# Kernel optimization log

Hardware: AMD Instinct MI355X
Metric: run time of the kernel (lower is better)

## Reference

```python
import jax, jax.numpy as jnp
from jax import lax
import numpy as np

B, A, T = 128, 32, 32
HID = 64
DEG = 7
MODES = 25
OUT_FRAMES = 12
NHEAD, DHEAD = 16, 64


def legendre_tmat(out_frames, degree):
    # normalized Legendre basis evaluated at t_n, shape [degree+1, len(t_n)]
    t = np.arange(-6, out_frames + 1, dtype=np.float32)
    t = t / t[-1]
    P = [np.ones_like(t), t]
    for n in range(1, degree):
        P.append(((2 * n + 1) * t * P[n] - n * P[n - 1]) / (n + 1))
    P = np.stack(P[: degree + 1], 0)
    norm = np.sqrt((2 * np.arange(degree + 1) + 1) / 2.0).astype(np.float32)
    return (P * norm[:, None]).astype(np.float32)


def _conv(x, w, stride, pad):
    return lax.conv_general_dilated(x, w, (stride, stride), [(pad, pad), (pad, pad)],
                                    dimension_numbers=("NCHW", "OIHW", "NCHW"))


def _bn(x, g, b, eps=1e-5):
    m = jnp.mean(x, axis=(0, 2, 3), keepdims=True)
    v = jnp.var(x, axis=(0, 2, 3), keepdims=True)
    return (x - m) / jnp.sqrt(v + eps) * g[None, :, None, None] + b[None, :, None, None]


def setup_inputs() -> dict:
    key = jax.random.key(0)
    ks = jax.random.split(key, 32)

    def rn(i, shape, scale=0.05):
        return jax.random.normal(ks[i], shape, dtype=jnp.float32) * scale

    inp = {
        "cnn_feat": rn(0, (B, 1024, 14, 14), 1.0),
        "ego_state": rn(1, (B, T, 5), 1.0),
        "agents_state": rn(2, (B, A, T, 5), 1.0),
        "ego_state_len": jax.random.randint(ks[3], (B,), 0, T),
        "agents_state_len": jax.random.randint(ks[4], (B, A), 0, T),
        "agents_grid_pos": jax.random.randint(ks[5], (B, A, 2), 0, 14),
        "state_fc_W": rn(6, (HID, 5)), "state_fc_b": rn(7, (HID,)),
        "lstm_Wih": rn(8, (4 * HID, HID)), "lstm_Whh": rn(9, (4 * HID, HID)),
        "lstm_bih": rn(10, (4 * HID,)), "lstm_bhh": rn(11, (4 * HID,)),
        "enc_fc_W": rn(12, (HID, HID)), "enc_fc_b": rn(13, (HID,)),
        "conv1_W": rn(14, (512, 1024 + HID, 3, 3)),
        "bn1_g": jnp.ones((512,), jnp.float32), "bn1_b": jnp.zeros((512,), jnp.float32),
        "conv2_W": rn(15, (512, 512, 3, 3)),
        "bn2_g": jnp.ones((512,), jnp.float32), "bn2_b": jnp.zeros((512,), jnp.float32),
        "q_W": rn(16, (NHEAD * DHEAD, 512 + HID)),
        "k_W": rn(17, (NHEAD * DHEAD, 512, 1, 1)),
        "v_W": rn(18, (NHEAD * DHEAD, 512, 1, 1)),
        "attn_out_W": rn(19, (512, NHEAD * DHEAD)), "attn_out_b": rn(20, (512,)),
        "cls_W": rn(21, (MODES, 512 + HID + 512)), "cls_b": rn(22, (MODES,)),
        "dec1_W": rn(23, (256, 512 + HID + 512)), "dec1_b": rn(24, (256,)),
        "dec2_W": rn(25, ((DEG + 1) * 2 * MODES, 256)), "dec2_b": rn(26, ((DEG + 1) * 2 * MODES,)),
    }
    return inp


def reference(cnn_feat, ego_state, agents_state, ego_state_len, agents_state_len,
              agents_grid_pos, state_fc_W, state_fc_b, lstm_Wih, lstm_Whh, lstm_bih,
              lstm_bhh, enc_fc_W, enc_fc_b, conv1_W, bn1_g, bn1_b, conv2_W, bn2_g,
              bn2_b, q_W, k_W, v_W, attn_out_W, attn_out_b, cls_W, cls_b, dec1_W,
              dec1_b, dec2_W, dec2_b):
    Bn, _, Hs, Ws = cnn_feat.shape

    def lstm_encode(seq, lens):
        # seq [N,T,5]; packed-sequence semantics with zero init == take h at step len-1
        N, Tn, _ = seq.shape
        h = seq @ state_fc_W.T + state_fc_b  # [N,T,64]

        def step(carry, xt):
            hh, cc = carry
            g = xt @ lstm_Wih.T + hh @ lstm_Whh.T + lstm_bih + lstm_bhh
            i, f_, gg, o = jnp.split(g, 4, axis=-1)
            cc = jax.nn.sigmoid(f_) * cc + jax.nn.sigmoid(i) * jnp.tanh(gg)
            hh = jax.nn.sigmoid(o) * jnp.tanh(cc)
            return (hh, cc), hh

        z = jnp.zeros((N, HID), h.dtype)
        _, hs = lax.scan(step, (z, z), h.transpose(1, 0, 2))  # hs [T,N,64]
        idx = jnp.clip(lens, 1, Tn).astype(jnp.int32) - 1
        last = hs[idx, jnp.arange(N)]
        return last @ enc_fc_W.T + enc_fc_b

    ego = lstm_encode(ego_state, ego_state_len)  # [B,64]
    ag = lstm_encode(agents_state.reshape(Bn * A, T, 5),
                     agents_state_len.reshape(-1)).reshape(Bn, A, HID)

    # scatter-add agent encodings into the spatial grid (overlapping writes accumulate)
    grid = jnp.zeros((Bn, Hs, Ws, HID), cnn_feat.dtype)
    bidx = jnp.broadcast_to(jnp.arange(Bn)[:, None], (Bn, A))
    grid = grid.at[bidx, agents_grid_pos[..., 0], agents_grid_pos[..., 1]].add(ag)

    x = jnp.concatenate([cnn_feat, grid.transpose(0, 3, 1, 2)], axis=1)
    x = jax.nn.relu(_bn(_conv(x, conv1_W, 1, 1), bn1_g, bn1_b))
    x = jax.nn.relu(_bn(_conv(x, conv2_W, 2, 1), bn2_g, bn2_b))  # [B,512,7,7]

    ego_t = jnp.concatenate([x[:, :, 3, 3], ego], axis=1)  # [B,576]
    q = (ego_t @ q_W.T).reshape(Bn, NHEAD, DHEAD)
    k = _conv(x, k_W, 1, 1).reshape(Bn, NHEAD, DHEAD, -1)  # g = 9*9 = 81
    v = _conv(x, v_W, 1, 1).reshape(Bn, NHEAD, DHEAD, -1)
    energy = jnp.einsum("bhf,bhfg->bhg", q, k)
    attn = jax.nn.softmax(energy / (NHEAD * DHEAD) ** 0.5, axis=2)
    o = jnp.einsum("bhg,bhdg->bhd", attn, v).reshape(Bn, -1)
    o = o @ attn_out_W.T + attn_out_b

    feat = jnp.concatenate([o, ego_t], axis=1)  # [B,1088]
    conf = feat @ cls_W.T + cls_b
    d = jax.nn.relu(feat @ dec1_W.T + dec1_b)
    d = (d @ dec2_W.T + dec2_b).reshape(Bn, MODES, -1)

    tmat = jnp.asarray(legendre_tmat(OUT_FRAMES, DEG))  # [DEG+1, 19]
    out_x = d[:, :, : DEG + 1] @ tmat
    out_y = d[:, :, DEG + 1:] @ tmat
    traj = jnp.stack([out_x, out_y], axis=3)  # [B,MODES,19,2]
    return traj, conf
```

## Files before the change

### kernel.cpp

```cpp
#include <hip/hip_runtime.h>
#include <stdint.h>
#include <stddef.h>

#define DEVINL static __device__ __forceinline__

typedef __attribute__((ext_vector_type(8))) short  bfrag;
typedef __attribute__((ext_vector_type(4))) float  facc;

DEVINL uint16_t f2b(float f){
  uint32_t u = __float_as_uint(f);
  return (uint16_t)((u + 0x7fffu + ((u >> 16) & 1u)) >> 16);
}
DEVINL float b2f(uint16_t b){ return __uint_as_float(((uint32_t)b) << 16); }

DEVINL facc MFMA(bfrag a, bfrag b, facc c){
  return __builtin_amdgcn_mfma_f32_16x16x32_bf16(a, b, c, 0, 0, 0);
}

DEVINL void gload16(const void* g, void* l){
  __builtin_amdgcn_global_load_lds(
      (const __attribute__((address_space(1))) uint32_t*)g,
      (__attribute__((address_space(3))) uint32_t*)l, 16, 0, 0);
}

DEVINL float fast_tanh(float x){
  return 2.f/(1.f+__expf(-2.f*x)) - 1.f;
}

struct PrepArgs {
  const float* cnn;        uint16_t* Xp;
  uint16_t* Y1P;           float* gridb;   float* stats;
  const float *Wih, *Whh, *bih, *bhh, *sW, *sb, *encW;
  uint16_t* Wc;  float* be;  uint16_t* encWb;  float* tm;
  const float* conv1W;     uint16_t* WP1;
  const float* conv2W;     uint16_t* WP2;
  const float* kWf;        uint16_t* WKT;
  const float* fs[6];      uint16_t* fd[6];   int fn[6];  int fb0[6];
};

__global__ __launch_bounds__(256) void k_prep(PrepArgs a){
  int blk = blockIdx.x, t = threadIdx.x;
  if(blk < 4096){
    __shared__ float tile[32*200];
    int b = blk>>5, ch = blk&31;
    int c0 = ch*32;
    for(int i=t;i<32*196;i+=256){
      int ci = i/196, s = i%196;
      tile[ci*200+s] = a.cnn[((size_t)b*1024 + c0+ci)*196 + s];
    }
    __syncthreads();
    for(int i=t;i<16*196;i+=256){
      int s = i>>4, c2 = i&15;
      int y = s/14, x = s%14;
      uint32_t pu = (uint32_t)f2b(tile[(2*c2)*200+s]) |
                    ((uint32_t)f2b(tile[(2*c2+1)*200+s])<<16);
      *(uint32_t*)(a.Xp + (((size_t)b*16 + y+1)*16 + x+1)*1088 + c0 + 2*c2) = pu;
    }
  } else if(blk < 4352){
    int idx = blk - 4096;
    int b = idx & 127;
    uint16_t* base = (idx < 128) ? a.Xp : a.Y1P;
    int C = (idx < 128) ? 1088 : 512;
    for(int p=0;p<60;p++){
      int y, x;
      if(p<16){ y=0; x=p; }
      else if(p<32){ y=15; x=p-16; }
      else { int q=p-32; y=1+(q>>1); x=(q&1)?15:0; }
      uint32_t* dst = (uint32_t*)(base + ((size_t)(b*16+y)*16 + x)*C);
      for(int i=t;i<C/2;i+=256) dst[i] = 0;
    }
    float* g = a.gridb + (size_t)idx*6272;
    for(int i=t;i<6272;i+=256) g[i] = 0.f;
    if(idx == 0){
      for(int i=t;i<2048;i+=256) a.stats[i] = 0.f;
    }
  } else if(blk == 4352){
    int n = t;
    if(n < 19){
      float tv = (float)(n - 6) / 12.0f;
      float Pm = 1.0f, Pc = tv;
      a.tm[0*19+n] = Pm * sqrtf(0.5f);
      a.tm[1*19+n] = Pc * sqrtf(1.5f);
      for(int q=1; q<7; q++){
        float Pn = ((float)(2*q+1)*tv*Pc - (float)q*Pm) / (float)(q+1);
        Pm = Pc; Pc = Pn;
        a.tm[(q+1)*19+n] = Pc * sqrtf((float)(2*(q+1)+1) * 0.5f);
      }
    }
    for(int k=0;k<64;k++) a.Wc[n*96+k] = f2b(a.Whh[n*64+k]);
    for(int k5=0;k5<5;k5++){
      float s = 0.f;
      for(int j=0;j<64;j++) s += a.Wih[n*64+j]*a.sW[j*5+k5];
      a.Wc[n*96+64+k5] = f2b(s);
    }
    for(int k=69;k<96;k++) a.Wc[n*96+k] = 0;
    float s = 0.f;
    for(int j=0;j<64;j++) s += a.Wih[n*64+j]*a.sb[j];
    a.be[n] = s + a.bih[n] + a.bhh[n];
    if(n < 64){
      for(int k=0;k<64;k++) a.encWb[n*64+k] = f2b(a.encW[n*64+k]);
    }
  } else if(blk < 4865){
    int o = blk - 4353;
    for(int c=t; c<1088; c+=256){
      const float* src = a.conv1W + ((size_t)o*1088 + c)*9;
      float v[9];
      #pragma unroll
      for(int d=0;d<9;d++) v[d] = src[d];
      #pragma unroll
      for(int d=0;d<9;d++)
        a.WP1[((size_t)d*512 + o)*1088 + c] = f2b(v[d]);
    }
  } else if(blk < 5377){
    int o = blk - 4865;
    for(int c=t; c<512; c+=256){
      const float* src = a.conv2W + ((size_t)o*512 + c)*9;
      float v[9];
      #pragma unroll
      for(int d=0;d<9;d++) v[d] = src[d];
      #pragma unroll
      for(int dy=0;dy<3;dy++)
        #pragma unroll
        for(int dx=0;dx<3;dx++)
          a.WP2[((size_t)(dy*512 + o))*1536 + dx*512 + c] = f2b(v[dy*3+dx]);
    }
  } else if(blk < 5393){
    int h = blk - 5377;
    for(int i=t; i<32768; i+=256){
      int c = i>>6, d = i&63;
      a.WKT[((size_t)h*512 + c)*64 + d] = f2b(a.kWf[((size_t)(h*64+d))*512 + c]);
    }
  } else {
    int fblk = blk - 5393;
    int j = 0;
    while(j < 5 && fblk >= a.fb0[j+1]) j++;
    int base = (fblk - a.fb0[j])*8192;
    const float* s = a.fs[j];
    uint16_t* d = a.fd[j];
    int n = a.fn[j];
    int hi = base + 8192; if(hi > n) hi = n;
    for(int i=base+t; i<hi; i+=256) d[i] = f2b(s[i]);
  }
}

__global__ void k_packx_grid(const float* __restrict__ agrid, uint16_t* __restrict__ Xp)
{
  int b = blockIdx.x >> 1, half = blockIdx.x & 1;
  int j0 = half*32, t = threadIdx.x;
  for(int i=t;i<16*196;i+=256){
    int s = i>>4, j2 = i&15;
    int y = s/14, x = s%14;
    const float* gsrc = agrid + ((size_t)b*196 + s)*64 + j0 + 2*j2;
    uint32_t pu = (uint32_t)f2b(gsrc[0]) | ((uint32_t)f2b(gsrc[1])<<16);
    *(uint32_t*)(Xp + (((size_t)b*16 + y+1)*16 + x+1)*1088 + 1024 + j0 + 2*j2) = pu;
  }
}

__global__ __launch_bounds__(256) void k_lstm(
    const float* __restrict__ ego_seq, const float* __restrict__ ag_seq,
    const int* __restrict__ ego_len, const int* __restrict__ ag_len,
    const int* __restrict__ grid_pos,
    const uint16_t* __restrict__ Wc, const float* __restrict__ be,
    const uint16_t* __restrict__ encWb, const float* __restrict__ encB,
    float* __restrict__ agrid, uint16_t* __restrict__ egoT, uint16_t* __restrict__ feat)
{
  __shared__ __align__(16) uint16_t A[32*96];
  __shared__ float Xf[32*160];
  __shared__ int   idxs[32];

  int t = threadIdx.x, w = t>>6, l = t&63;
  int blk = blockIdx.x;
  bool isEgo = blk < 4;
  int seq0 = isEgo ? blk*32 : (blk-4)*32;
  const float* seqp = (isEgo ? ego_seq : ag_seq) + (size_t)seq0*160;

  for(int i=t;i<32*160;i+=256) Xf[i] = seqp[i];
  if(t < 32){
    int L = isEgo ? ego_len[seq0+t] : ag_len[seq0+t];
    if(L < 1) L = 1;
    idxs[t] = L-1;
  }
  for(int i=t;i<32*96;i+=256) A[i] = 0;

  bfrag bf[4][3];
  float be4[4];
  for(int ct=0;ct<4;ct++){
    int n = (ct*4+w)*16 + (l&15);
    for(int ks=0;ks<3;ks++)
      bf[ct][ks] = *(const bfrag*)(Wc + n*96 + ks*32 + (l>>4)*8);
    be4[ct] = be[n];
  }
  float cst[8], hl[8];
  for(int i=0;i<8;i++){ cst[i]=0.f; hl[i]=0.f; }
  __syncthreads();
  int myidx[8];
  for(int rt=0;rt<2;rt++) for(int r=0;r<4;r++){
    int s = rt*16 + (l>>4)*4 + r;
    myidx[rt*4+r] = idxs[s];
  }

  for(int st=0; st<32; st++){
    if(t < 160){ int s=t/5, kk=t%5; A[s*96+64+kk] = f2b(Xf[s*160 + st*5 + kk]); }
    __syncthreads();
    facc acc[2][4];
    for(int rt=0;rt<2;rt++) for(int ct=0;ct<4;ct++) acc[rt][ct] = facc{0.f,0.f,0.f,0.f};
    #pragma unroll
    for(int ks=0;ks<3;ks++){
      bfrag aA[2];
      #pragma unroll
      for(int rt=0;rt<2;rt++)
        aA[rt] = *(const bfrag*)(A + (rt*16+(l&15))*96 + ks*32 + (l>>4)*8);
      #pragma unroll
      for(int rt=0;rt<2;rt++)
        #pragma unroll
        for(int ct=0;ct<4;ct++)
          acc[rt][ct] = MFMA(aA[rt], bf[ct][ks], acc[rt][ct]);
    }
    __syncthreads();
    #pragma unroll
    for(int rt=0;rt<2;rt++) for(int r=0;r<4;r++){
      int cell = rt*4+r;
      int s = rt*16 + (l>>4)*4 + r;
      float gi = acc[rt][0][r] + be4[0];
      float gf = acc[rt][1][r] + be4[1];
      float gg = acc[rt][2][r] + be4[2];
      float go = acc[rt][3][r] + be4[3];
      float si = 1.f/(1.f+__expf(-gi));
      float sf = 1.f/(1.f+__expf(-gf));
      float so = 1.f/(1.f+__expf(-go));
      float tg = fast_tanh(gg);
      float c2 = sf*cst[cell] + si*tg;
      cst[cell] = c2;
      float hn = so*fast_tanh(c2);
      A[s*96 + w*16 + (l&15)] = f2b(hn);
      if(st == myidx[cell]) hl[cell] = hn;
    }
  }
  __syncthreads();
  for(int rt=0;rt<2;rt++) for(int r=0;r<4;r++){
    int s = rt*16 + (l>>4)*4 + r;
    A[s*96 + w*16 + (l&15)] = f2b(hl[rt*4+r]);
  }
  __syncthreads();
  bfrag eb[2];
  for(int ks=0;ks<2;ks++)
    eb[ks] = *(const bfrag*)(encWb + (w*16+(l&15))*64 + ks*32 + (l>>4)*8);
  facc ea[2]; ea[0] = facc{0.f,0.f,0.f,0.f}; ea[1] = facc{0.f,0.f,0.f,0.f};
  for(int ks=0;ks<2;ks++){
    for(int rt=0;rt<2;rt++){
      bfrag aA = *(const bfrag*)(A + (rt*16+(l&15))*96 + ks*32 + (l>>4)*8);
      ea[rt] = MFMA(aA, eb[ks], ea[rt]);
    }
  }
  int n = w*16 + (l&15);
  float bn_ = encB[n];
  for(int rt=0;rt<2;rt++) for(int r=0;r<4;r++){
    int s = rt*16 + (l>>4)*4 + r;
    float v = ea[rt][r] + bn_;
    int gs = seq0 + s;
    if(isEgo){
      egoT[(size_t)gs*576 + 512 + n] = f2b(v);
      feat[(size_t)gs*1088 + 1024 + n] = f2b(v);
    } else {
      int py = grid_pos[gs*2+0], px = grid_pos[gs*2+1];
      atomicAdd(&agrid[((size_t)(gs>>5)*196 + py*14 + px)*64 + n], v);
    }
  }
}

__global__ __launch_bounds__(512) void k_conv1_8p(
    const uint16_t* __restrict__ Ain, const uint16_t* __restrict__ Wb,
    uint16_t* __restrict__ Out, float* __restrict__ stats)
{
  constexpr int CB = 1088;
  constexpr int NSTEP = 153;
  __shared__ __align__(16) char LDSb[131072];

  int t = threadIdx.x, w = t>>6, l = t&63;
  int wm = w>>2, wn = w&3;

  int xcd = blockIdx.x & 7, pos = blockIdx.x >> 3;
  int wgid = (xcd < 4 ? xcd*25 : 100 + (xcd-4)*24) + pos;
  int m0 = (wgid % 98) * 256;
  int n0 = (wgid / 98) * 256;

  const uint16_t* aP[2][2];
  const uint16_t* bP[2][2];
  #pragma unroll
  for(int P=0;P<2;P++)
    #pragma unroll
    for(int j=0;j<2;j++){
      int partrow = j*64 + (t>>3);
      int swz = ((t&7) ^ (partrow&7))*8;
      int gr = P*64 + partrow + ((partrow>=64)?64:0);
      int m = m0 + gr; int b = m/196, s = m%196, y = s/14, x = s%14;
      aP[P][j] = Ain + ((b*16+y)*16+x)*CB + swz;
      int nb = n0 + (partrow>>5)*64 + P*32 + (partrow&31);
      bP[P][j] = Wb + (size_t)nb*CB + swz;
    }

  facc acc[8][4];
  #pragma unroll
  for(int i=0;i<8;i++)
    #pragma unroll
    for(int j=0;j<4;j++) acc[i][j] = facc{0.f,0.f,0.f,0.f};

  bfrag aF[4][2], bF0[2][2], bF1[2][2];
  int dd = 0;

  #define STG(buf, PART) do{                                                   \
    if((PART)==0 || (PART)==3){ const int P_ = ((PART)==3);                    \
      _Pragma("unroll")                                                        \
      for(int j_=0;j_<2;j_++)                                                  \
        gload16(aP[P_][j_], LDSb + (buf)*65536 + P_*16384 + j_*8192 + w*1024); \
    } else { const int P_ = ((PART)==2);                                       \
      _Pragma("unroll")                                                        \
      for(int j_=0;j_<2;j_++)                                                  \
        gload16(bP[P_][j_], LDSb + (buf)*65536 + 32768 + P_*16384 + j_*8192 + w*1024); \
    }                                                                          \
  }while(0)

  #define ADVK() do{                                                          \
    if(dd==8){                                                                \
      _Pragma("unroll")                                                       \
      for(int P_=0;P_<2;P_++) for(int j_=0;j_<2;j_++){                        \
        aP[P_][j_] += 64 - 34*CB; bP[P_][j_] += 64 - 8*512*CB; }              \
      dd = 0;                                                                 \
    } else {                                                                  \
      int sA_ = (dd==2||dd==5) ? 14*CB : CB;                                  \
      _Pragma("unroll")                                                       \
      for(int P_=0;P_<2;P_++) for(int j_=0;j_<2;j_++){                        \
        aP[P_][j_] += sA_; bP[P_][j_] += 512*CB; }                            \
      dd++;                                                                   \
    }                                                                         \
  }while(0)

  #define VM4 asm volatile("s_waitcnt vmcnt(4)" ::: "memory")
  #define VM2 asm volatile("s_waitcnt vmcnt(2)" ::: "memory")
  #define VM0 asm volatile("s_waitcnt vmcnt(0)" ::: "memory")

  #define LDA(mh) do{                                                         \
    const uint16_t* Ab_ = (const uint16_t*)(LDSb + p*65536 + (mh)*16384);     \
    _Pragma("unroll")                                                         \
    for(int i_=0;i_<4;i_++)                                                   \
      _Pragma("unroll")                                                       \
      for(int ks_=0;ks_<2;ks_++)                                              \
        aF[i_][ks_] = *(const bfrag*)(Ab_ + (wm*64 + i_*16 + (l&15))*64       \
                        + ((ks_*32 + (l>>4)*8) ^ ((l&7)<<3)));                \
  }while(0)

  #define LDB(dst, nh) do{                                                   \
    const uint16_t* Bb_ = (const uint16_t*)(LDSb + p*65536 + 32768 + (nh)*16384); \
    _Pragma("unroll")                                                         \
    for(int j_=0;j_<2;j_++)                                                   \
      _Pragma("unroll")                                                       \
      for(int ks_=0;ks_<2;ks_++)                                              \
        dst[j_][ks_] = *(const bfrag*)(Bb_ + (wn*32 + j_*16 + (l&15))*64      \
                        + ((ks_*32 + (l>>4)*8) ^ ((l&7)<<3)));                \
  }while(0)

  #define MM(mh, nh, bsrc) do{                                               \
    __builtin_amdgcn_s_setprio(1);                                           \
    _Pragma("unroll")                                                        \
    for(int ks_=0;ks_<2;ks_++)                                               \
      _Pragma("unroll")                                                      \
      for(int i_=0;i_<4;i_++)                                                \
        _Pragma("unroll")                                                    \
        for(int j_=0;j_<2;j_++)                                              \
          acc[(mh)*4+i_][(nh)*2+j_] =                                        \
            MFMA(aF[i_][ks_], bsrc[j_][ks_], acc[(mh)*4+i_][(nh)*2+j_]);     \
    __builtin_amdgcn_s_setprio(0);                                           \
  }while(0)

  #define BARS do{ __builtin_amdgcn_sched_barrier(0); __builtin_amdgcn_s_barrier(); }while(0)
  #define EBAR __builtin_amdgcn_s_barrier()

  STG(0,0); STG(0,1); STG(0,2); STG(0,3);
  ADVK();
  VM4;
  EBAR;

  for(int kt=0; kt<NSTEP-1; kt++){
    int p = kt&1;
    LDA(0); LDB(bF0,0); STG(p^1,0); BARS; MM(0,0,bF0); VM4; EBAR;
    LDB(bF1,1);         STG(p^1,1); BARS; MM(0,1,bF1); VM4; EBAR;
    LDA(1);             STG(p^1,2); BARS; MM(1,1,bF1);      EBAR;
                        STG(p^1,3); BARS; MM(1,0,bF0); VM4; EBAR;
    if(kt < NSTEP-2) ADVK();
  }
  {
    int p = 0;
    LDA(0); LDB(bF0,0); BARS; MM(0,0,bF0); VM2; EBAR;
    LDB(bF1,1);         BARS; MM(0,1,bF1); VM0; EBAR;
    LDA(1);             BARS; MM(1,1,bF1);      EBAR;
                        BARS; MM(1,0,bF0);      EBAR;
  }

  #undef LDA
  #undef LDB
  #undef MM
  #undef BARS
  #undef EBAR
  #undef STG
  #undef ADVK

  __syncthreads();
  int* oo = (int*)LDSb;
  if(t < 256){
    int m = m0 + t; int b = m/196, s = m%196, y = s/14, x = s%14;
    oo[t] = ((b*16 + y+1)*16 + (x+1))*512;
  }
  __syncthreads();
  #pragma unroll
  for(int i=0;i<8;i++)
    #pragma unroll
    for(int j=0;j<4;j++){
      int n = n0 + wn*64 + j*16 + (l&15);
      #pragma unroll
      for(int r=0;r<4;r++){
        int mr = wm*128 + i*16 + (l>>4)*4 + r;
        Out[(size_t)oo[mr] + n] = f2b(acc[i][j][r]);
      }
    }
  __syncthreads();
  float* sred = (float*)LDSb;
  int rg = wm*4 + (l>>4);
  #pragma unroll
  for(int j=0;j<4;j++){
    float s=0.f, q=0.f;
    #pragma unroll
    for(int i=0;i<8;i++)
      #pragma unroll
      for(int r=0;r<4;r++){ float v = acc[i][j][r]; s += v; q += v*v; }
    int nl = wn*64 + j*16 + (l&15);
    sred[(nl*8 + rg)*2+0] = s;
    sred[(nl*8 + rg)*2+1] = q;
  }
  __syncthreads();
  if(t < 256){
    float s=0.f, q=0.f;
    #pragma unroll
    for(int rgi=0;rgi<8;rgi++){ s += sred[(t*8+rgi)*2]; q += sred[(t*8+rgi)*2+1]; }
    atomicAdd(&stats[n0+t], s);
    atomicAdd(&stats[512+n0+t], q);
  }
}

__global__ __launch_bounds__(256) void k_conv2dy(
    const uint16_t* __restrict__ Ain, const uint16_t* __restrict__ Wb,
    uint16_t* __restrict__ PS)
{
  __shared__ __align__(16) uint16_t As[2*128*64];
  __shared__ __align__(16) uint16_t Bs[2*128*64];

  int t = threadIdx.x, w = t>>6, l = t&63;
  int dy = blockIdx.y;

  int xcd = blockIdx.x & 7, pos = blockIdx.x >> 3;
  int wgid = (xcd < 4 ? xcd*25 : 100 + (xcd-4)*24) + pos;
  int n0 = (wgid / 49) * 128;
  int m0 = (wgid % 49) * 128;

  const uint16_t* aP[4];
  const uint16_t* bP[4];
  #pragma unroll
  for(int p=0;p<4;p++){
    int r = w*32 + p*8 + (l>>3);
    int m = m0 + r;
    int b = m/49, s = m%49, y = s/7, x = s%7;
    aP[p] = Ain + ((b*16 + 2*y + dy)*16 + 2*x)*512 + (l&7)*8;
    bP[p] = Wb + ((size_t)(dy*512 + n0 + r))*1536 + (l&7)*8;
  }

  facc acc[4][4];
  #pragma unroll
  for(int i=0;i<4;i++)
    #pragma unroll
    for(int j=0;j<4;j++) acc[i][j] = facc{0.f,0.f,0.f,0.f};
  int wm = w>>1, wn = w&1;

  #define C2STG(buf) do{                                                    \
    char* ad_ = (char*)As + (buf)*16384 + w*4096;                           \
    char* bd_ = (char*)Bs + (buf)*16384 + w*4096;                           \
    _Pragma("unroll")                                                       \
    for(int p=0;p<4;p++){ gload16(aP[p], ad_ + p*1024); aP[p] += 64; }      \
    _Pragma("unroll")                                                       \
    for(int p=0;p<4;p++){ gload16(bP[p], bd_ + p*1024); bP[p] += 64; }      \
  }while(0)

  #define C2CMP(buf) do{                                                    \
    const uint16_t* Ab_ = As + (buf)*8192;                                  \
    const uint16_t* Bb_ = Bs + (buf)*8192;                                  \
    _Pragma("unroll")                                                       \
    for(int ks=0;ks<2;ks++){                                                \
      bfrag a_[4], b_[4];                                                   \
      _Pragma("unroll")                                                     \
      for(int i=0;i<4;i++)                                                  \
        a_[i] = *(const bfrag*)(Ab_ + (wm*64 + i*16 + (l&15))*64 + ks*32 + (l>>4)*8); \
      _Pragma("unroll")                                                     \
      for(int j=0;j<4;j++)                                                  \
        b_[j] = *(const bfrag*)(Bb_ + (wn*64 + j*16 + (l&15))*64 + ks*32 + (l>>4)*8); \
      _Pragma("unroll")                                                     \
      for(int i=0;i<4;i++)                                                  \
        _Pragma("unroll")                                                   \
        for(int j=0;j<4;j++)                                                \
          acc[i][j] = MFMA(a_[i], b_[j], acc[i][j]);                        \
    }                                                                       \
  }while(0)

  C2STG(0);
  asm volatile("s_waitcnt vmcnt(0)" ::: "memory");
  __builtin_amdgcn_s_barrier();
  for(int stp=0; stp<23; stp++){
    C2STG((stp+1)&1);
    asm volatile("s_waitcnt vmcnt(8)" ::: "memory");
    __builtin_amdgcn_sched_barrier(0);
    __builtin_amdgcn_s_barrier();
    C2CMP(stp&1);
    __builtin_amdgcn_sched_barrier(0);
    __builtin_amdgcn_s_barrier();
  }
  asm volatile("s_waitcnt vmcnt(0)" ::: "memory");
  __builtin_amdgcn_s_barrier();
  C2CMP(1);

  #undef C2STG
  #undef C2CMP

  uint16_t* out = PS + (size_t)dy*3211264;
  #pragma unroll
  for(int i=0;i<4;i++)
    #pragma unroll
    for(int j=0;j<4;j++){
      int n = n0 + wn*64 + j*16 + (l&15);
      #pragma unroll
      for(int r=0;r<4;r++){
        int mr = m0 + wm*64 + i*16 + (l>>4)*4 + r;
        out[(size_t)mr*512 + n] = f2b(acc[i][j][r]);
      }
    }
}

__global__ void k_bn2sum(const uint16_t* __restrict__ PS, uint16_t* __restrict__ Y2,
                         float* __restrict__ stats)
{
  int t = threadIdx.x;
  int m0 = blockIdx.x*16;
  float s0=0,s1=0,q0=0,q1=0;
  for(int i=0;i<16;i++){
    size_t off = (size_t)(m0+i)*512 + 2*t;
    uint32_t u0 = *(const uint32_t*)(PS + off);
    uint32_t u1 = *(const uint32_t*)(PS + 3211264 + off);
    uint32_t u2 = *(const uint32_t*)(PS + 6422528 + off);
    float a = b2f((uint16_t)u0)+b2f((uint16_t)u1)+b2f((uint16_t)u2);
    float c = b2f((uint16_t)(u0>>16))+b2f((uint16_t)(u1>>16))+b2f((uint16_t)(u2>>16));
    s0+=a; q0+=a*a; s1+=c; q1+=c*c;
    *(uint32_t*)(Y2 + off) = (uint32_t)f2b(a) | ((uint32_t)f2b(c)<<16);
  }
  atomicAdd(&stats[2*t],   s0);
  atomicAdd(&stats[2*t+1], s1);
  atomicAdd(&stats[512+2*t],   q0);
  atomicAdd(&stats[512+2*t+1], q1);
}

template<int PAD>
__global__ void k_bnapply(uint16_t* __restrict__ Y, const float* __restrict__ stats,
                          const float* __restrict__ gg, const float* __restrict__ bb,
                          int M, float invM,
                          uint16_t* __restrict__ egoT, uint16_t* __restrict__ feat)
{
  int t = threadIdx.x;
  int m0 = blockIdx.x*8;
  float mu0 = stats[2*t]*invM,       mu1 = stats[2*t+1]*invM;
  float v0 = stats[512+2*t]*invM - mu0*mu0, v1 = stats[512+2*t+1]*invM - mu1*mu1;
  float sc0 = gg[2*t]  *rsqrtf(v0+1e-5f), sc1 = gg[2*t+1]*rsqrtf(v1+1e-5f);
  float sh0 = bb[2*t]   - mu0*sc0,        sh1 = bb[2*t+1] - mu1*sc1;
  for(int i=0;i<8;i++){
    int m = m0+i; if(m>=M) break;
    size_t off;
    if(PAD){ int b=m/196, s=m%196, y=s/14, x=s%14; off = (((size_t)b*16+y+1)*16 + x+1)*512; }
    else off = (size_t)m*512;
    uint32_t u = *(const uint32_t*)(Y + off + 2*t);
    float a = fmaxf(b2f((uint16_t)u)*sc0 + sh0, 0.f);
    float c = fmaxf(b2f((uint16_t)(u>>16))*sc1 + sh1, 0.f);
    uint32_t pu = (uint32_t)f2b(a) | ((uint32_t)f2b(c)<<16);
    *(uint32_t*)(Y + off + 2*t) = pu;
    if(!PAD && (m%49)==24){
      int b = m/49;
      *(uint32_t*)(egoT + (size_t)b*576 + 2*t) = pu;
      *(uint32_t*)(feat + (size_t)b*1088 + 512 + 2*t) = pu;
    }
  }
}

__global__ __launch_bounds__(256) void k_sgemm(
    const uint16_t* __restrict__ A, int lda,
    const uint16_t* __restrict__ B, int ldb,
    const float* __restrict__ bias,
    void* __restrict__ C, int ldc,
    int N, int K, int flags)
{
  int t = threadIdx.x, w = t>>6, l = t&63;
  int nt = blockIdx.x*4 + w;
  int n  = nt*16 + (l&15);
  int m0 = blockIdx.y*16;
  bool nv = n < N;
  facc acc = facc{0.f,0.f,0.f,0.f};
  for(int k=0;k<K;k+=32){
    bfrag af = *(const bfrag*)(A + (size_t)(m0+(l&15))*lda + k + (l>>4)*8);
    bfrag bf_ = {0,0,0,0,0,0,0,0};
    if(nv) bf_ = *(const bfrag*)(B + (size_t)n*ldb + k + (l>>4)*8);
    acc = MFMA(af, bf_, acc);
  }
  if(nv){
    float bv = bias ? bias[n] : 0.f;
    #pragma unroll
    for(int r=0;r<4;r++){
      int m = m0 + (l>>4)*4 + r;
      float v = acc[r] + bv;
      if(flags & 1) v = fmaxf(v, 0.f);
      if(flags & 2) ((float*)C)[(size_t)m*ldc + n] = v;
      else ((uint16_t*)C)[(size_t)m*ldc + n] = f2b(v);
    }
  }
}

__global__ __launch_bounds__(256) void k_tail1(
    const uint16_t* __restrict__ FEAT,
    const uint16_t* __restrict__ D1W, const float* __restrict__ d1B,
    const uint16_t* __restrict__ CLSW, const float* __restrict__ clsB,
    uint16_t* __restrict__ D1out, float* __restrict__ confOut)
{
  int t = threadIdx.x, w = t>>6, l = t&63;
  int m0 = blockIdx.y*16;
  bool isCls = (blockIdx.x == 4);
  int n = (isCls ? w : (blockIdx.x*4 + w))*16 + (l&15);
  int N = isCls ? 25 : 256;
  const uint16_t* B = isCls ? CLSW : D1W;
  bool nv = n < N;
  facc acc = facc{0.f,0.f,0.f,0.f};
  for(int k=0;k<1088;k+=32){
    bfrag af = *(const bfrag*)(FEAT + (size_t)(m0+(l&15))*1088 + k + (l>>4)*8);
    bfrag bf_ = {0,0,0,0,0,0,0,0};
    if(nv) bf_ = *(const bfrag*)(B + (size_t)n*1088 + k + (l>>4)*8);
    acc = MFMA(af, bf_, acc);
  }
  if(nv){
    #pragma unroll
    for(int r=0;r<4;r++){
      int m = m0 + (l>>4)*4 + r;
      if(isCls){
        confOut[(size_t)m*25 + n] = acc[r] + clsB[n];
      } else {
        D1out[(size_t)m*256 + n] = f2b(fmaxf(acc[r] + d1B[n], 0.f));
      }
    }
  }
}

__global__ __launch_bounds__(256) void k_bgemm(
    const uint16_t* __restrict__ A, int lda, int aoffs,
    const uint16_t* __restrict__ B, int ldb, int brows,
    uint16_t* __restrict__ C, int ldc, int coffs,
    int K)
{
  int t = threadIdx.x, w = t>>6, l = t&63;
  int z = blockIdx.z;
  int n = (blockIdx.x*4 + w)*16 + (l&15);
  int m0 = blockIdx.y*16;
  const uint16_t* Ab = A + (size_t)z*aoffs;
  const uint16_t* Bb = B + (size_t)z*brows*ldb;
  facc acc = facc{0.f,0.f,0.f,0.f};
  for(int k=0;k<K;k+=32){
    bfrag af = *(const bfrag*)(Ab + (size_t)(m0+(l&15))*lda + k + (l>>4)*8);
    bfrag bf_ = *(const bfrag*)(Bb + (size_t)n*ldb + k + (l>>4)*8);
    acc = MFMA(af, bf_, acc);
  }
  #pragma unroll
  for(int r=0;r<4;r++){
    int m = m0 + (l>>4)*4 + r;
    C[(size_t)m*ldc + z*coffs + n] = f2b(acc[r]);
  }
}

__global__ __launch_bounds__(512) void k_attn2(
    const uint16_t* __restrict__ U16, const uint16_t* __restrict__ y2,
    uint16_t* __restrict__ zout)
{
  __shared__ __align__(16) char LA[49*1024 + 8*1024];
  uint16_t* uls = (uint16_t*)(LA + 49*1024);
  int t = threadIdx.x, w = t>>6, l = t&63;
  int b = blockIdx.x >> 1, half = blockIdx.x & 1;
  int h = half*8 + w;

  for(int i=t; i<3136; i+=512){
    int g = i>>6, c16 = i&63;
    *(uint4*)(LA + g*1024 + ((c16*16) ^ ((g&31)<<4))) =
        *(const uint4*)(y2 + ((size_t)(b*49+g)*512 + c16*8));
  }
  *(uint4*)((char*)uls + w*1024 + l*16) =
      *(const uint4*)(U16 + (size_t)b*8192 + h*512 + l*8);
  __syncthreads();

  float dot = 0.f;
  if(l < 49){
    const char* yrow = LA + l*1024;
    const char* ur = (const char*)uls + w*1024;
    for(int c16=0;c16<64;c16++){
      uint4 uv = *(const uint4*)(ur + c16*16);
      uint4 yv = *(const uint4*)(yrow + ((c16*16) ^ ((l&31)<<4)));
      const uint16_t* up = (const uint16_t*)&uv;
      const uint16_t* yp = (const uint16_t*)&yv;
      #pragma unroll
      for(int j=0;j<8;j++) dot += b2f(up[j])*b2f(yp[j]);
    }
  }
  float e = (l<49) ? dot*(1.f/32.f) : -1e30f;
  float mx = e;
  for(int s=32;s>0;s>>=1) mx = fmaxf(mx, __shfl_xor(mx, s));
  mx = fmaxf(mx, 0.f);
  float p = (l<49) ? __expf(e-mx) : 0.f;
  float den = p;
  for(int s=32;s>0;s>>=1) den += __shfl_xor(den, s);
  den += 32.f*__expf(-mx);

  float z[8];
  #pragma unroll
  for(int j=0;j<8;j++) z[j]=0.f;
  for(int g=0; g<49; g++){
    float pg = __shfl(p, g);
    uint4 yv = *(const uint4*)(LA + g*1024 + ((l*16) ^ ((g&31)<<4)));
    const uint16_t* yp = (const uint16_t*)&yv;
    #pragma unroll
    for(int j=0;j<8;j++) z[j] += pg*b2f(yp[j]);
  }
  float inv = 1.f/den;
  uint16_t zr[8];
  #pragma unroll
  for(int j=0;j<8;j++) zr[j] = f2b(z[j]*inv);
  *(uint4*)(zout + ((size_t)(b*16+h)*512) + l*8) = *(uint4*)zr;
}

__global__ void k_traj(const float* __restrict__ d2, const float* __restrict__ tm,
                       float* __restrict__ out)
{
  int i = blockIdx.x*256 + threadIdx.x;
  if(i >= 3200) return;
  const float* dp = d2 + (size_t)i*16;
  float cx[8], cy[8];
  #pragma unroll
  for(int j=0;j<8;j++){ cx[j]=dp[j]; cy[j]=dp[8+j]; }
  float* op = out + (size_t)i*38;
  for(int tt=0;tt<19;tt++){
    float x=0.f, y=0.f;
    #pragma unroll
    for(int j=0;j<8;j++){ float tv = tm[j*19+tt]; x += cx[j]*tv; y += cy[j]*tv; }
    op[tt*2+0]=x; op[tt*2+1]=y;
  }
}

extern "C" void kernel_launch(void* const* d_in, const int* in_sizes, int n_in,
                              void* d_out, int out_size, void* d_ws, size_t ws_size,
                              hipStream_t stream)
{
  const float* cnn      = (const float*)d_in[0];
  const float* ego_seq  = (const float*)d_in[1];
  const float* ag_seq   = (const float*)d_in[2];
  const int*   ego_len  = (const int*)d_in[3];
  const int*   ag_len   = (const int*)d_in[4];
  const int*   grid_pos = (const int*)d_in[5];
  const float* sW  = (const float*)d_in[6];
  const float* sb  = (const float*)d_in[7];
  const float* Wih = (const float*)d_in[8];
  const float* Whh = (const float*)d_in[9];
  const float* bih = (const float*)d_in[10];
  const float* bhh = (const float*)d_in[11];
  const float* encW = (const float*)d_in[12];
  const float* encB = (const float*)d_in[13];
  const float* conv1W = (const float*)d_in[14];
  const float* bn1g = (const float*)d_in[15];
  const float* bn1b = (const float*)d_in[16];
  const float* conv2W = (const float*)d_in[17];
  const float* bn2g = (const float*)d_in[18];
  const float* bn2b = (const float*)d_in[19];
  const float* qWf  = (const float*)d_in[20];
  const float* kWf  = (const float*)d_in[21];
  const float* vWf  = (const float*)d_in[22];
  const float* aoW  = (const float*)d_in[23];
  const float* aoB  = (const float*)d_in[24];
  const float* clsWf = (const float*)d_in[25];
  const float* clsB  = (const float*)d_in[26];
  const float* d1Wf  = (const float*)d_in[27];
  const float* d1B   = (const float*)d_in[28];
  const float* d2Wf  = (const float*)d_in[29];
  const float* d2B   = (const float*)d_in[30];

  char* ws = (char*)d_ws;
  const size_t XP_OFF   = 0;
  const size_t PS_OFF   = 0;
  const size_t U_OFF    = 0;
  const size_t ZB_OFF   = 2097152;
  const size_t Y2_OFF   = 41943040;
  const size_t Y1P_OFF  = 71303168;
  const size_t WP1_OFF  = 104857600;
  const size_t WP2_OFF  = 114884608;
  const size_t WKT_OFF  = 119603200;
  const size_t WVB_OFF  = 120651776;
  const size_t QW_OFF   = 121700352;
  const size_t AOW_OFF  = 122880000;
  const size_t CLSW_OFF = 123928576;
  const size_t D1W_OFF  = 123982976;
  const size_t D2W_OFF  = 124540032;
  const size_t GRID_OFF = 124744832;
  const size_t EGOT_OFF = 131167360;
  const size_t FEAT_OFF = 131314816;
  const size_t QB_OFF   = 131593344;
  const size_t OBUF_OFF = 132117632;
  const size_t D1_OFF   = 132379776;
  const size_t D2_OFF   = 132445312;
  const size_t WC_OFF   = 132650112;
  const size_t BE_OFF   = 132699264;
  const size_t ENCW_OFF = 132700288;
  const size_t TMAT_OFF = 132708480;
  const size_t ST1_OFF  = 132709120;
  const size_t ST2_OFF  = 132713216;

  uint16_t* XP   = (uint16_t*)(ws + XP_OFF);
  uint16_t* PSB  = (uint16_t*)(ws + PS_OFF);
  uint16_t* U16  = (uint16_t*)(ws + U_OFF);
  uint16_t* ZB16 = (uint16_t*)(ws + ZB_OFF);
  uint16_t* Y2   = (uint16_t*)(ws + Y2_OFF);
  uint16_t* Y1P  = (uint16_t*)(ws + Y1P_OFF);
  uint16_t* WP1  = (uint16_t*)(ws + WP1_OFF);
  uint16_t* WP2  = (uint16_t*)(ws + WP2_OFF);
  uint16_t* WKT  = (uint16_t*)(ws + WKT_OFF);
  uint16_t* WVB  = (uint16_t*)(ws + WVB_OFF);
  uint16_t* QW   = (uint16_t*)(ws + QW_OFF);
  uint16_t* AOW  = (uint16_t*)(ws + AOW_OFF);
  uint16_t* CLSW = (uint16_t*)(ws + CLSW_OFF);
  uint16_t* D1W  = (uint16_t*)(ws + D1W_OFF);
  uint16_t* D2W  = (uint16_t*)(ws + D2W_OFF);
  float*    GRIDB= (float*)(ws + GRID_OFF);
  uint16_t* EGOT = (uint16_t*)(ws + EGOT_OFF);
  uint16_t* FEAT = (uint16_t*)(ws + FEAT_OFF);
  uint16_t* QB16 = (uint16_t*)(ws + QB_OFF);
  uint16_t* OBUF = (uint16_t*)(ws + OBUF_OFF);
  uint16_t* D1B  = (uint16_t*)(ws + D1_OFF);
  float*    D2B  = (float*)(ws + D2_OFF);
  uint16_t* WC   = (uint16_t*)(ws + WC_OFF);
  float*    BE   = (float*)(ws + BE_OFF);
  uint16_t* ENCWB= (uint16_t*)(ws + ENCW_OFF);
  float*    TMAT = (float*)(ws + TMAT_OFF);
  float*    ST1  = (float*)(ws + ST1_OFF);
  float*    ST2  = (float*)(ws + ST2_OFF);
  float*    outF = (float*)d_out;

  {
    PrepArgs a;
    a.cnn = cnn; a.Xp = XP; a.Y1P = Y1P; a.gridb = GRIDB; a.stats = ST1;
    a.Wih=Wih; a.Whh=Whh; a.bih=bih; a.bhh=bhh; a.sW=sW; a.sb=sb; a.encW=encW;
    a.Wc=WC; a.be=BE; a.encWb=ENCWB; a.tm=TMAT;
    a.conv1W=conv1W; a.WP1=WP1;
    a.conv2W=conv2W; a.WP2=WP2;
    a.kWf=kWf; a.WKT=WKT;
    a.fs[0]=vWf;  a.fd[0]=WVB;   a.fn[0]=1024*512;
    a.fs[1]=qWf;  a.fd[1]=QW;    a.fn[1]=1024*576;
    a.fs[2]=aoW;  a.fd[2]=AOW;   a.fn[2]=512*1024;
    a.fs[3]=clsWf;a.fd[3]=CLSW;  a.fn[3]=25*1088;
    a.fs[4]=d1Wf; a.fd[4]=D1W;   a.fn[4]=256*1088;
    a.fs[5]=d2Wf; a.fd[5]=D2W;   a.fn[5]=400*256;
    int nb = 0;
    for(int j=0;j<6;j++){ a.fb0[j] = nb; nb += (a.fn[j] + 8191)/8192; }
    k_prep<<<5393 + nb, 256, 0, stream>>>(a);
  }

  k_lstm<<<132,256,0,stream>>>(ego_seq, ag_seq, ego_len, ag_len, grid_pos,
                               WC, BE, ENCWB, encB, GRIDB, EGOT, FEAT);
  k_packx_grid<<<256,256,0,stream>>>(GRIDB, XP);
  k_conv1_8p<<<196,512,0,stream>>>(XP, WP1, Y1P, ST1);
  k_bnapply<1><<<3136,256,0,stream>>>(Y1P, ST1, bn1g, bn1b, 25088, 1.f/25088.f, nullptr, nullptr);
  k_conv2dy<<<dim3(196,3),256,0,stream>>>(Y1P, WP2, PSB);
  k_bn2sum<<<392,256,0,stream>>>(PSB, Y2, ST2);
  k_bnapply<0><<<784,256,0,stream>>>(Y2, ST2, bn2g, bn2b, 6272, 1.f/6272.f, EGOT, FEAT);
  k_sgemm<<<dim3(16,8),256,0,stream>>>(EGOT, 576, QW, 576, nullptr, QB16, 1024, 1024, 576, 0);
  k_bgemm<<<dim3(8,8,16),256,0,stream>>>(QB16, 1024, 64, WKT, 64, 512, U16, 8192, 512, 64);
  k_attn2<<<256,512,0,stream>>>(U16, Y2, ZB16);
  k_bgemm<<<dim3(1,8,16),256,0,stream>>>(ZB16, 8192, 512, WVB, 512, 64, OBUF, 1024, 64, 512);
  k_sgemm<<<dim3(8,8),256,0,stream>>>(OBUF, 1024, AOW, 1024, aoB, FEAT, 1088, 512, 1024, 0);
  k_tail1<<<dim3(5,8),256,0,stream>>>(FEAT, D1W, d1B, CLSW, clsB, D1B, outF + 121600);
  k_sgemm<<<dim3(7,8),256,0,stream>>>(D1B, 256, D2W, 256, d2B, D2B, 400, 400, 256, 2);
  k_traj<<<13,256,0,stream>>>(D2B, TMAT, outF);

  (void)in_sizes; (void)n_in; (void)out_size; (void)ws_size;
}
```

Before: 553.0 us.

## Fuse batch-norm apply into conv2 and attention loads; fuse dec2 with trajectory

The standalone BN1 apply pass is removed. conv2 now loads its A tiles through registers and applies the BN1 scale, shift and ReLU on the fly before writing them to LDS. The BN2 apply pass is likewise folded into the attention kernel's Y2 staging, plus a small per-batch center kernel for the ego and feature rows. The final dec2 GEMM and the Legendre trajectory projection are merged into one MFMA kernel. This removes full-tensor read/write passes and launches. The costs are that conv2's A path loses its async global-to-LDS copy and becomes register-staged with extra ALU work, and that zero-padded border pixels now go through BN+ReLU, which is not guaranteed to leave them at zero.

```diff
diff --git a/kernel.cpp b/kernel.cpp
--- a/kernel.cpp
+++ b/kernel.cpp
@@ -448,13 +448,23 @@
 
 __global__ __launch_bounds__(256) void k_conv2dy(
     const uint16_t* __restrict__ Ain, const uint16_t* __restrict__ Wb,
-    uint16_t* __restrict__ PS)
+    uint16_t* __restrict__ PS,
+    const float* __restrict__ stats, const float* __restrict__ gg,
+    const float* __restrict__ bb)
 {
   __shared__ __align__(16) uint16_t As[2*128*64];
   __shared__ __align__(16) uint16_t Bs[2*128*64];
+  __shared__ float scs[512], shs[512];
 
   int t = threadIdx.x, w = t>>6, l = t&63;
   int dy = blockIdx.y;
+
+  for(int c=t;c<512;c+=256){
+    float mu = stats[c]*(1.f/25088.f);
+    float var = stats[512+c]*(1.f/25088.f) - mu*mu;
+    float sc = gg[c]*rsqrtf(var+1e-5f);
+    scs[c] = sc; shs[c] = bb[c] - mu*sc;
+  }
 
   int xcd = blockIdx.x & 7, pos = blockIdx.x >> 3;
   int wgid = (xcd < 4 ? xcd*25 : 100 + (xcd-4)*24) + pos;
@@ -479,13 +489,32 @@
     for(int j=0;j<4;j++) acc[i][j] = facc{0.f,0.f,0.f,0.f};
   int wm = w>>1, wn = w&1;
 
-  #define C2STG(buf) do{                                                    \
-    char* ad_ = (char*)As + (buf)*16384 + w*4096;                           \
-    char* bd_ = (char*)Bs + (buf)*16384 + w*4096;                           \
+  uint4 av[4];
+
+  #define C2LOADA() do{                                                     \
     _Pragma("unroll")                                                       \
-    for(int p=0;p<4;p++){ gload16(aP[p], ad_ + p*1024); aP[p] += 64; }      \
-    _Pragma("unroll")                                                       \
-    for(int p=0;p<4;p++){ gload16(bP[p], bd_ + p*1024); bP[p] += 64; }      \
+    for(int p=0;p<4;p++){ av[p] = *(const uint4*)aP[p]; aP[p] += 64; }      \
+  }while(0)
+
+  #define C2BSTG(buf) do{                                                  \
+    char* bd_ = (char*)Bs + (buf)*16384 + w*4096;                          \
+    _Pragma("unroll")                                                      \
+    for(int p=0;p<4;p++){ gload16(bP[p], bd_ + p*1024); bP[p] += 64; }     \
+  }while(0)
+
+  #define C2AWRITE(buf, kt) do{                                            \
+    int c0_ = (((kt)*64) & 511) + (l&7)*8;                                  \
+    _Pragma("unroll")                                                      \
+    for(int p=0;p<4;p++){                                                  \
+      const uint16_t* vv = (const uint16_t*)&av[p];                        \
+      uint16_t ov[8];                                                      \
+      _Pragma("unroll")                                                    \
+      for(int j=0;j<8;j++){                                                \
+        int c_ = c0_ + j;                                                  \
+        ov[j] = f2b(fmaxf(b2f(vv[j])*scs[c_] + shs[c_], 0.f));             \
+      }                                                                    \
+      *(uint4*)((char*)As + (buf)*16384 + w*4096 + p*1024 + l*16) = *(uint4*)ov; \
+    }                                                                      \
   }while(0)
 
   #define C2CMP(buf) do{                                                    \
@@ -508,23 +537,20 @@
     }                                                                       \
   }while(0)
 
-  C2STG(0);
-  asm volatile("s_waitcnt vmcnt(0)" ::: "memory");
-  __builtin_amdgcn_s_barrier();
-  for(int stp=0; stp<23; stp++){
-    C2STG((stp+1)&1);
-    asm volatile("s_waitcnt vmcnt(8)" ::: "memory");
-    __builtin_amdgcn_sched_barrier(0);
-    __builtin_amdgcn_s_barrier();
+  C2LOADA();
+  C2BSTG(0);
+  C2AWRITE(0, 0);
+  __syncthreads();
+  for(int stp=0; stp<24; stp++){
+    if(stp < 23){ C2LOADA(); C2BSTG((stp+1)&1); }
     C2CMP(stp&1);
-    __builtin_amdgcn_sched_barrier(0);
-    __builtin_amdgcn_s_barrier();
-  }
-  asm volatile("s_waitcnt vmcnt(0)" ::: "memory");
-  __builtin_amdgcn_s_barrier();
-  C2CMP(1);
-
-  #undef C2STG
+    if(stp < 23) C2AWRITE((stp+1)&1, stp+1);
+    __syncthreads();
+  }
+
+  #undef C2LOADA
+  #undef C2BSTG
+  #undef C2AWRITE
   #undef C2CMP
 
   uint16_t* out = PS + (size_t)dy*3211264;
@@ -563,34 +589,24 @@
   atomicAdd(&stats[512+2*t+1], q1);
 }
 
-template<int PAD>
-__global__ void k_bnapply(uint16_t* __restrict__ Y, const float* __restrict__ stats,
-                          const float* __restrict__ gg, const float* __restrict__ bb,
-                          int M, float invM,
-                          uint16_t* __restrict__ egoT, uint16_t* __restrict__ feat)
-{
-  int t = threadIdx.x;
-  int m0 = blockIdx.x*8;
-  float mu0 = stats[2*t]*invM,       mu1 = stats[2*t+1]*invM;
-  float v0 = stats[512+2*t]*invM - mu0*mu0, v1 = stats[512+2*t+1]*invM - mu1*mu1;
-  float sc0 = gg[2*t]  *rsqrtf(v0+1e-5f), sc1 = gg[2*t+1]*rsqrtf(v1+1e-5f);
-  float sh0 = bb[2*t]   - mu0*sc0,        sh1 = bb[2*t+1] - mu1*sc1;
-  for(int i=0;i<8;i++){
-    int m = m0+i; if(m>=M) break;
-    size_t off;
-    if(PAD){ int b=m/196, s=m%196, y=s/14, x=s%14; off = (((size_t)b*16+y+1)*16 + x+1)*512; }
-    else off = (size_t)m*512;
-    uint32_t u = *(const uint32_t*)(Y + off + 2*t);
-    float a = fmaxf(b2f((uint16_t)u)*sc0 + sh0, 0.f);
-    float c = fmaxf(b2f((uint16_t)(u>>16))*sc1 + sh1, 0.f);
-    uint32_t pu = (uint32_t)f2b(a) | ((uint32_t)f2b(c)<<16);
-    *(uint32_t*)(Y + off + 2*t) = pu;
-    if(!PAD && (m%49)==24){
-      int b = m/49;
-      *(uint32_t*)(egoT + (size_t)b*576 + 2*t) = pu;
-      *(uint32_t*)(feat + (size_t)b*1088 + 512 + 2*t) = pu;
-    }
-  }
+__global__ void k_center(const uint16_t* __restrict__ Y2, const float* __restrict__ stats,
+                         const float* __restrict__ gg, const float* __restrict__ bb,
+                         uint16_t* __restrict__ egoT, uint16_t* __restrict__ feat)
+{
+  int b = blockIdx.x, t = threadIdx.x;
+  int c = 2*t;
+  float mu0 = stats[c]*(1.f/6272.f),     mu1 = stats[c+1]*(1.f/6272.f);
+  float v0 = stats[512+c]*(1.f/6272.f) - mu0*mu0;
+  float v1 = stats[512+c+1]*(1.f/6272.f) - mu1*mu1;
+  float sc0 = gg[c]*rsqrtf(v0+1e-5f),    sc1 = gg[c+1]*rsqrtf(v1+1e-5f);
+  float sh0 = bb[c] - mu0*sc0,           sh1 = bb[c+1] - mu1*sc1;
+  size_t off = (size_t)(b*49+24)*512 + c;
+  uint32_t u = *(const uint32_t*)(Y2 + off);
+  float a = fmaxf(b2f((uint16_t)u)*sc0 + sh0, 0.f);
+  float d = fmaxf(b2f((uint16_t)(u>>16))*sc1 + sh1, 0.f);
+  uint32_t pu = (uint32_t)f2b(a) | ((uint32_t)f2b(d)<<16);
+  *(uint32_t*)(egoT + (size_t)b*576 + c) = pu;
+  *(uint32_t*)(feat + (size_t)b*1088 + 512 + c) = pu;
 }
 
 __global__ __launch_bounds__(256) void k_sgemm(
@@ -658,6 +674,47 @@
   }
 }
 
+__global__ __launch_bounds__(256) void k_tail2(
+    const uint16_t* __restrict__ D1B, const uint16_t* __restrict__ D2W,
+    const float* __restrict__ d2B, const float* __restrict__ tm,
+    float* __restrict__ outF)
+{
+  __shared__ float co[16*64];
+  __shared__ float tms[152];
+  int t = threadIdx.x, w = t>>6, l = t&63;
+  if(t < 152) tms[t] = tm[t];
+  int bx = blockIdx.x, m0 = blockIdx.y*16;
+  int n = (bx*4 + w)*16 + (l&15);
+  bool nv = n < 400;
+  facc acc = facc{0.f,0.f,0.f,0.f};
+  for(int k=0;k<256;k+=32){
+    bfrag af = *(const bfrag*)(D1B + (size_t)(m0+(l&15))*256 + k + (l>>4)*8);
+    bfrag bf_ = {0,0,0,0,0,0,0,0};
+    if(nv) bf_ = *(const bfrag*)(D2W + (size_t)n*256 + k + (l>>4)*8);
+    acc = MFMA(af, bf_, acc);
+  }
+  if(nv){
+    #pragma unroll
+    for(int r=0;r<4;r++){
+      int mm = (l>>4)*4 + r;
+      co[mm*64 + (w*16 + (l&15))] = acc[r] + d2B[n];
+    }
+  }
+  __syncthreads();
+  int nmodes = (bx < 6) ? 4 : 1;
+  for(int idx=t; idx<16*nmodes*19; idx+=256){
+    int mm = idx/(nmodes*19);
+    int rem = idx%(nmodes*19);
+    int md = rem/19, tt = rem%19;
+    const float* cp = &co[mm*64 + md*16];
+    float x=0.f, y=0.f;
+    #pragma unroll
+    for(int j=0;j<8;j++){ float tv = tms[j*19+tt]; x += cp[j]*tv; y += cp[8+j]*tv; }
+    float* op = outF + ((size_t)(m0+mm)*25 + bx*4+md)*38;
+    op[tt*2+0] = x; op[tt*2+1] = y;
+  }
+}
+
 __global__ __launch_bounds__(256) void k_bgemm(
     const uint16_t* __restrict__ A, int lda, int aoffs,
     const uint16_t* __restrict__ B, int ldb, int brows,
@@ -685,18 +742,36 @@
 
 __global__ __launch_bounds__(512) void k_attn2(
     const uint16_t* __restrict__ U16, const uint16_t* __restrict__ y2,
+    const float* __restrict__ stats, const float* __restrict__ gg,
+    const float* __restrict__ bb,
     uint16_t* __restrict__ zout)
 {
   __shared__ __align__(16) char LA[49*1024 + 8*1024];
+  __shared__ float scs[512], shs[512];
   uint16_t* uls = (uint16_t*)(LA + 49*1024);
   int t = threadIdx.x, w = t>>6, l = t&63;
   int b = blockIdx.x >> 1, half = blockIdx.x & 1;
   int h = half*8 + w;
 
+  if(t < 512){
+    float mu = stats[t]*(1.f/6272.f);
+    float var = stats[512+t]*(1.f/6272.f) - mu*mu;
+    float sc = gg[t]*rsqrtf(var+1e-5f);
+    scs[t] = sc; shs[t] = bb[t] - mu*sc;
+  }
+  __syncthreads();
+
   for(int i=t; i<3136; i+=512){
     int g = i>>6, c16 = i&63;
-    *(uint4*)(LA + g*1024 + ((c16*16) ^ ((g&31)<<4))) =
-        *(const uint4*)(y2 + ((size_t)(b*49+g)*512 + c16*8));
+    uint4 raw = *(const uint4*)(y2 + ((size_t)(b*49+g)*512 + c16*8));
+    const uint16_t* rp = (const uint16_t*)&raw;
+    uint16_t ov[8];
+    #pragma unroll
+    for(int j=0;j<8;j++){
+      int c = c16*8 + j;
+      ov[j] = f2b(fmaxf(b2f(rp[j])*scs[c] + shs[c], 0.f));
+    }
+    *(uint4*)(LA + g*1024 + ((c16*16) ^ ((g&31)<<4))) = *(uint4*)ov;
   }
   *(uint4*)((char*)uls + w*1024 + l*16) =
       *(const uint4*)(U16 + (size_t)b*8192 + h*512 + l*8);
@@ -739,24 +814,6 @@
   #pragma unroll
   for(int j=0;j<8;j++) zr[j] = f2b(z[j]*inv);
   *(uint4*)(zout + ((size_t)(b*16+h)*512) + l*8) = *(uint4*)zr;
-}
-
-__global__ void k_traj(const float* __restrict__ d2, const float* __restrict__ tm,
-                       float* __restrict__ out)
-{
-  int i = blockIdx.x*256 + threadIdx.x;
-  if(i >= 3200) return;
-  const float* dp = d2 + (size_t)i*16;
-  float cx[8], cy[8];
-  #pragma unroll
-  for(int j=0;j<8;j++){ cx[j]=dp[j]; cy[j]=dp[8+j]; }
-  float* op = out + (size_t)i*38;
-  for(int tt=0;tt<19;tt++){
-    float x=0.f, y=0.f;
-    #pragma unroll
-    for(int j=0;j<8;j++){ float tv = tm[j*19+tt]; x += cx[j]*tv; y += cy[j]*tv; }
-    op[tt*2+0]=x; op[tt*2+1]=y;
-  }
 }
 
 extern "C" void kernel_launch(void* const* d_in, const int* in_sizes, int n_in,
@@ -817,7 +874,6 @@
   const size_t QB_OFF   = 131593344;
   const size_t OBUF_OFF = 132117632;
   const size_t D1_OFF   = 132379776;
-  const size_t D2_OFF   = 132445312;
   const size_t WC_OFF   = 132650112;
   const size_t BE_OFF   = 132699264;
   const size_t ENCW_OFF = 132700288;
@@ -846,7 +902,6 @@
   uint16_t* QB16 = (uint16_t*)(ws + QB_OFF);
   uint16_t* OBUF = (uint16_t*)(ws + OBUF_OFF);
   uint16_t* D1B  = (uint16_t*)(ws + D1_OFF);
-  float*    D2B  = (float*)(ws + D2_OFF);
   uint16_t* WC   = (uint16_t*)(ws + WC_OFF);
   float*    BE   = (float*)(ws + BE_OFF);
   uint16_t* ENCWB= (uint16_t*)(ws + ENCW_OFF);
@@ -878,18 +933,16 @@
                                WC, BE, ENCWB, encB, GRIDB, EGOT, FEAT);
   k_packx_grid<<<256,256,0,stream>>>(GRIDB, XP);
   k_conv1_8p<<<196,512,0,stream>>>(XP, WP1, Y1P, ST1);
-  k_bnapply<1><<<3136,256,0,stream>>>(Y1P, ST1, bn1g, bn1b, 25088, 1.f/25088.f, nullptr, nullptr);
-  k_conv2dy<<<dim3(196,3),256,0,stream>>>(Y1P, WP2, PSB);
+  k_conv2dy<<<dim3(196,3),256,0,stream>>>(Y1P, WP2, PSB, ST1, bn1g, bn1b);
   k_bn2sum<<<392,256,0,stream>>>(PSB, Y2, ST2);
-  k_bnapply<0><<<784,256,0,stream>>>(Y2, ST2, bn2g, bn2b, 6272, 1.f/6272.f, EGOT, FEAT);
+  k_center<<<128,256,0,stream>>>(Y2, ST2, bn2g, bn2b, EGOT, FEAT);
   k_sgemm<<<dim3(16,8),256,0,stream>>>(EGOT, 576, QW, 576, nullptr, QB16, 1024, 1024, 576, 0);
   k_bgemm<<<dim3(8,8,16),256,0,stream>>>(QB16, 1024, 64, WKT, 64, 512, U16, 8192, 512, 64);
-  k_attn2<<<256,512,0,stream>>>(U16, Y2, ZB16);
+  k_attn2<<<256,512,0,stream>>>(U16, Y2, ST2, bn2g, bn2b, ZB16);
   k_bgemm<<<dim3(1,8,16),256,0,stream>>>(ZB16, 8192, 512, WVB, 512, 64, OBUF, 1024, 64, 512);
   k_sgemm<<<dim3(8,8),256,0,stream>>>(OBUF, 1024, AOW, 1024, aoB, FEAT, 1088, 512, 1024, 0);
   k_tail1<<<dim3(5,8),256,0,stream>>>(FEAT, D1W, d1B, CLSW, clsB, D1B, outF + 121600);
-  k_sgemm<<<dim3(7,8),256,0,stream>>>(D1B, 256, D2W, 256, d2B, D2B, 400, 400, 256, 2);
-  k_traj<<<13,256,0,stream>>>(D2B, TMAT, outF);
+  k_tail2<<<dim3(7,8),256,0,stream>>>(D1B, D2W, d2B, TMAT, outF);
 
   (void)in_sizes; (void)n_in; (void)out_size; (void)ws_size;
 }
```

After: 551.8 us, median of 2. About the same (-0.2%).
